# Optimization experiments

Hardware: AMD Instinct MI355X
Metric: run time of the kernel (lower is better)

The kernel has to match this reference:

```python
import jax, jax.numpy as jnp
import numpy as np

B, P, M, C = 64, 8732, 16, 81
THRESHOLD = 0.5
NEG_POS_RATIO = 3
ALPHA = 1.0  # config.reg_weights
EPS = 1e-7


def cxcy_to_xy(c):
    return jnp.concatenate([c[..., :2] - c[..., 2:] / 2.0,
                            c[..., :2] + c[..., 2:] / 2.0], axis=-1)


def _rand_boxes_cxcy(key, shape):
    k1, k2 = jax.random.split(key)
    cxcy = jax.random.uniform(k1, shape + (2,), minval=0.2, maxval=0.8)
    wh = jax.random.uniform(k2, shape + (2,), minval=0.05, maxval=0.35)
    return jnp.concatenate([cxcy, wh], axis=-1)


def setup_inputs() -> dict:
    key = jax.random.key(0)
    ks = jax.random.split(key, 5)
    predicted_locs = cxcy_to_xy(_rand_boxes_cxcy(ks[0], (B, P)))          # valid corner boxes
    predicted_scores = jax.random.normal(ks[1], (B, P, C), dtype=jnp.float32)
    boxes = jnp.clip(cxcy_to_xy(_rand_boxes_cxcy(ks[2], (B, M))), 0.0, 1.0)  # GT corner boxes
    labels = jax.random.randint(ks[3], (B, M), 1, C)                       # object labels (1..C-1)
    priors_cxcy = _rand_boxes_cxcy(ks[4], (P,))
    return {"predicted_locs": predicted_locs, "predicted_scores": predicted_scores,
            "boxes": boxes, "labels": labels, "priors_cxcy": priors_cxcy}


def jaccard(a, b):
    # a: [M,4], b: [P,4] corner boxes -> [M,P] IoU
    lt = jnp.maximum(a[:, None, :2], b[None, :, :2])
    rb = jnp.minimum(a[:, None, 2:], b[None, :, 2:])
    wh = jnp.clip(rb - lt, 0.0)
    inter = wh[..., 0] * wh[..., 1]
    area_a = (a[:, 2] - a[:, 0]) * (a[:, 3] - a[:, 1])
    area_b = (b[:, 2] - b[:, 0]) * (b[:, 3] - b[:, 1])
    return inter / (area_a[:, None] + area_b[None, :] - inter)


def diou_loss(b1, b2):
    # corner boxes, elementwise over leading dims -> per-box loss 1 - DIoU
    lt = jnp.maximum(b1[..., :2], b2[..., :2])
    rb = jnp.minimum(b1[..., 2:], b2[..., 2:])
    wh = jnp.clip(rb - lt, 0.0)
    inter = wh[..., 0] * wh[..., 1]
    area1 = (b1[..., 2] - b1[..., 0]) * (b1[..., 3] - b1[..., 1])
    area2 = (b2[..., 2] - b2[..., 0]) * (b2[..., 3] - b2[..., 1])
    iou = inter / (area1 + area2 - inter + EPS)
    c1 = (b1[..., :2] + b1[..., 2:]) / 2.0
    c2 = (b2[..., :2] + b2[..., 2:]) / 2.0
    inter_diag = jnp.sum((c1 - c2) ** 2, axis=-1)
    enc_lt = jnp.minimum(b1[..., :2], b2[..., :2])
    enc_rb = jnp.maximum(b1[..., 2:], b2[..., 2:])
    outer_diag = jnp.sum((enc_rb - enc_lt) ** 2, axis=-1)
    dious = jnp.clip(iou - inter_diag / (outer_diag + EPS), -1.0, 1.0)
    return 1.0 - dious


def reference(predicted_locs, predicted_scores, boxes, labels, priors_cxcy):
    priors_xy = cxcy_to_xy(priors_cxcy)

    def assign(boxes_i, labels_i):
        overlap = jaccard(boxes_i, priors_xy)              # [M, P]
        ovl_prior = overlap.max(axis=0)                    # best overlap per prior
        obj_prior = overlap.argmax(axis=0)                 # best object per prior
        ovl_obj = overlap.max(axis=1)                      # best overlap per object
        prior_obj = overlap.argmax(axis=1)                 # best prior per object
        valid = ovl_obj > 0
        j_idx = jnp.cumsum(valid.astype(jnp.int32)) - 1    # index within filtered list (faithful)
        idx = jnp.where(valid, prior_obj, P)               # P -> dropped (out of bounds)
        ovl_prior = ovl_prior.at[idx].set(1.0, mode='drop')
        obj_prior = obj_prior.at[idx].set(j_idx, mode='drop')
        lab = labels_i[obj_prior]
        label_pos = jnp.where(ovl_prior < THRESHOLD, 0, lab)
        label_neg = jnp.where(ovl_prior < THRESHOLD - 0.1, -1, lab)
        return label_pos, label_neg

    true_classes, true_neg_classes = jax.vmap(assign)(boxes, labels)  # [B,P] each
    positive = true_classes > 0                                        # [B,P]
    pos_f = positive.astype(jnp.float32)
    n_pos_total = jnp.sum(pos_f)

    # Localization loss: DIoU(pred_pos, pred_pos) with reduce='mean' (faithful to source)
    per_box = diou_loss(predicted_locs, predicted_locs)                # [B,P]
    loc_loss = jnp.sum(per_box * pos_f) / jnp.maximum(n_pos_total, 1.0)

    # Confidence loss: per-prior CE + hard-negative mining (neg_pos_ratio)
    logp = jax.nn.log_softmax(predicted_scores, axis=-1)
    conf_all = -jnp.take_along_axis(logp, true_classes[..., None], axis=-1)[..., 0]  # [B,P]
    conf_pos_sum = jnp.sum(conf_all * pos_f)
    conf_neg = jnp.where(positive, 0.0, conf_all)
    conf_neg_sorted = -jnp.sort(-conf_neg, axis=-1)                    # descending
    n_hard = NEG_POS_RATIO * jnp.sum(positive, axis=1)                 # [B]
    hard_mask = (jnp.arange(P)[None, :] < n_hard[:, None]).astype(jnp.float32)
    conf_loss = (jnp.sum(conf_neg_sorted * hard_mask) + conf_pos_sum) / n_pos_total

    return conf_loss + ALPHA * loc_loss
```

## Files before the change

### kernel.cpp

```cpp
#include <hip/hip_runtime.h>
#include <math.h>

#define B_ 64
#define P_ 8732
#define M_ 16
#define C_ 81
#define THRESH 0.5f
#define EPS_ 1e-7f

#define CE_GRID 768
#define NBLK_CE CE_GRID
#define ROWS_PER_CHUNK 64
#define NCHUNKS ((B_ * P_) / ROWS_PER_CHUNK)
#define CHUNK_F4 (ROWS_PER_CHUNK * C_ / 4)

__global__ __launch_bounds__(1024) void assign_kernel(
    const float* __restrict__ boxes,
    const int*   __restrict__ labels,
    const float* __restrict__ priors,
    int*         __restrict__ true_classes,
    int*         __restrict__ n_pos)
{
    const int b = blockIdx.x;
    const int tid = threadIdx.x;
    const int lane = tid & 63;
    const int wv = tid >> 6;

    __shared__ float s_ovl[P_];
    __shared__ unsigned char s_obj[P_];
    __shared__ float s_bx[M_][4];
    __shared__ float s_barea[M_];
    __shared__ int   s_lab[M_];
    __shared__ float s_wv[M_][16];
    __shared__ int   s_wp[M_][16];
    __shared__ float s_ovl_obj[M_];
    __shared__ int   s_prior_obj[M_];
    __shared__ int   s_cnt[16];

    if (tid < M_*4) ((float*)s_bx)[tid] = boxes[b*M_*4 + tid];
    if (tid < M_)   s_lab[tid] = labels[b*M_ + tid];
    __syncthreads();
    if (tid < M_)
        s_barea[tid] = (s_bx[tid][2]-s_bx[tid][0])*(s_bx[tid][3]-s_bx[tid][1]);
    __syncthreads();

    float bestv[M_]; int bestp[M_];
    #pragma unroll
    for (int m = 0; m < M_; ++m) { bestv[m] = -1.0f; bestp[m] = 0x7fffffff; }

    for (int p = tid; p < P_; p += 1024) {
        float4 pc = ((const float4*)priors)[p];
        float px1 = pc.x - pc.z*0.5f, py1 = pc.y - pc.w*0.5f;
        float px2 = pc.x + pc.z*0.5f, py2 = pc.y + pc.w*0.5f;
        float parea = (px2-px1)*(py2-py1);
        float bv = -1.0f; int bm = 0;
        #pragma unroll
        for (int m = 0; m < M_; ++m) {
            float ix1 = fmaxf(s_bx[m][0], px1);
            float iy1 = fmaxf(s_bx[m][1], py1);
            float ix2 = fminf(s_bx[m][2], px2);
            float iy2 = fminf(s_bx[m][3], py2);
            float iw = fmaxf(ix2-ix1, 0.0f);
            float ih = fmaxf(iy2-iy1, 0.0f);
            float inter = iw*ih;
            float iou = inter / (s_barea[m] + parea - inter);
            if (iou > bv) { bv = iou; bm = m; }
            if (iou > bestv[m]) { bestv[m] = iou; bestp[m] = p; }
        }
        s_ovl[p] = bv;
        s_obj[p] = (unsigned char)bm;
    }

    #pragma unroll
    for (int m = 0; m < M_; ++m) {
        float v = bestv[m]; int p = bestp[m];
        #pragma unroll
        for (int o = 32; o; o >>= 1) {
            float v2 = __shfl_xor(v, o);
            int   p2 = __shfl_xor(p, o);
            if (v2 > v || (v2 == v && p2 < p)) { v = v2; p = p2; }
        }
        if (lane == 0) { s_wv[m][wv] = v; s_wp[m][wv] = p; }
    }
    __syncthreads();

    if (tid < M_) {
        float v = s_wv[tid][0]; int p = s_wp[tid][0];
        #pragma unroll
        for (int w = 1; w < 16; ++w) {
            float v2 = s_wv[tid][w]; int p2 = s_wp[tid][w];
            if (v2 > v || (v2 == v && p2 < p)) { v = v2; p = p2; }
        }
        s_ovl_obj[tid] = v; s_prior_obj[tid] = p;
    }
    __syncthreads();

    if (tid == 0) {
        int cnt = 0;
        for (int m = 0; m < M_; ++m) {
            if (s_ovl_obj[m] > 0.0f) {
                int p = s_prior_obj[m];
                s_ovl[p] = 1.0f;
                s_obj[p] = (unsigned char)cnt;
                cnt++;
            }
        }
    }
    __syncthreads();

    int cpos = 0;
    for (int p = tid; p < P_; p += 1024) {
        int tc = 0;
        if (!(s_ovl[p] < THRESH)) tc = s_lab[s_obj[p]];
        true_classes[(size_t)b*P_ + p] = tc;
        cpos += (tc > 0);
    }
    #pragma unroll
    for (int o = 32; o; o >>= 1) cpos += __shfl_xor(cpos, o);
    if (lane == 0) s_cnt[wv] = cpos;
    __syncthreads();
    if (tid == 0) {
        int t = 0;
        #pragma unroll
        for (int w = 0; w < 16; ++w) t += s_cnt[w];
        n_pos[b] = t;
    }
}

__device__ __forceinline__ void ce_stage_load(const float4* __restrict__ scores4,
                                              int c, int tid, float4 st4[6])
{
    const float4* src = scores4 + (size_t)c * CHUNK_F4;
    #pragma unroll
    for (int k = 0; k < 5; ++k) st4[k] = src[k*256 + tid];
    if (tid < 16) st4[5] = src[1280 + tid];
}

__device__ __forceinline__ void ce_stage_write(float* bufp, int tid,
                                               const float4 st4[6])
{
    float4* dst = (float4*)bufp;
    #pragma unroll
    for (int k = 0; k < 5; ++k) dst[k*256 + tid] = st4[k];
    if (tid < 16) dst[1280 + tid] = st4[5];
}

__global__ __launch_bounds__(256) void ce_loc_kernel(
    const float* __restrict__ scores,
    const float* __restrict__ locs,
    const int*   __restrict__ tcls,
    float*       __restrict__ conf_neg,
    float*       __restrict__ blk_pos,
    float*       __restrict__ blk_loc)
{
    const int tid  = threadIdx.x;
    const int lane = tid & 63;
    const int wv   = tid >> 6;
    const int s    = lane & 3;
    const int rl   = (lane >> 2) + wv * 16;

    __shared__ __attribute__((aligned(16))) float s_buf[2][ROWS_PER_CHUNK * C_];
    __shared__ float s_red[4][2];

    const int cnt   = (s == 0) ? 21 : 20;
    const int cbase = (s == 0) ? 0  : (1 + 20 * s);

    float p_acc = 0.f, l_acc = 0.f;
    const float4* scores4 = (const float4*)scores;

    float4 st4[6];

    int c0 = blockIdx.x;
    ce_stage_load(scores4, c0, tid, st4);
    ce_stage_write(s_buf[0], tid, st4);
    __syncthreads();

    int buf = 0;
    for (int c = c0; c < NCHUNKS; c += CE_GRID) {
        const int cn = c + CE_GRID;
        const bool have_next = (cn < NCHUNKS);
        if (have_next) ce_stage_load(scores4, cn, tid, st4);

        const float* rowp = &s_buf[buf][rl * C_ + cbase];
        float x[21];
        float mx = -INFINITY;
        #pragma unroll
        for (int k = 0; k < 21; ++k) {
            if (k < cnt) { x[k] = rowp[k]; mx = fmaxf(mx, x[k]); }
            else x[k] = -INFINITY;
        }
        mx = fmaxf(mx, __shfl_xor(mx, 1));
        mx = fmaxf(mx, __shfl_xor(mx, 2));

        const int row = c * ROWS_PER_CHUNK + rl;
        const int t = tcls[row];

        float e = 0.f, stv = 0.f;
        #pragma unroll
        for (int k = 0; k < 21; ++k) {
            e += __expf(x[k] - mx);
            if ((cbase + k == t) && (k < cnt)) stv = x[k];
        }
        e   += __shfl_xor(e, 1);   e   += __shfl_xor(e, 2);
        stv += __shfl_xor(stv, 1); stv += __shfl_xor(stv, 2);

        if (s == 0) {
            float conf = mx + __logf(e) - stv;
            if (t > 0) {
                conf_neg[row] = 0.f;
                p_acc += conf;
                float4 bx = ((const float4*)locs)[row];
                float w = bx.z - bx.x, h = bx.w - bx.y;
                float iw = fmaxf(w, 0.f), ih = fmaxf(h, 0.f);
                float inter = iw * ih;
                float area  = w * h;
                float iou   = inter / (area + area - inter + EPS_);
                float diou  = fminf(fmaxf(iou, -1.f), 1.f);
                l_acc += 1.f - diou;
            } else {
                conf_neg[row] = fmaxf(conf, 0.f);
            }
        }

        if (have_next) ce_stage_write(s_buf[buf ^ 1], tid, st4);
        __syncthreads();
        buf ^= 1;
    }

    #pragma unroll
    for (int o = 32; o; o >>= 1) {
        p_acc += __shfl_xor(p_acc, o);
        l_acc += __shfl_xor(l_acc, o);
    }
    if (lane == 0) { s_red[wv][0] = p_acc; s_red[wv][1] = l_acc; }
    __syncthreads();
    if (tid == 0) {
        blk_pos[blockIdx.x] = s_red[0][0] + s_red[1][0] + s_red[2][0] + s_red[3][0];
        blk_loc[blockIdx.x] = s_red[0][1] + s_red[1][1] + s_red[2][1] + s_red[3][1];
    }
}

__global__ __launch_bounds__(1024) void topk_kernel(
    const float* __restrict__ conf_neg,
    const int*   __restrict__ n_pos,
    float*       __restrict__ hard)
{
    const int b = blockIdx.x;
    const int tid = threadIdx.x;
    const int lane = tid & 63;
    const int wv = tid >> 6;

    __shared__ float s_v[P_];
    __shared__ int   s_hist[16][256];
    __shared__ int   s_cg[257];
    __shared__ int   s_sel;
    __shared__ int   s_t[16];
    __shared__ float s_f[16];

    for (int i = tid; i < P_; i += 1024) s_v[i] = conf_neg[(size_t)b*P_ + i];
    int k = 3 * n_pos[b];
    if (k <= 0) { if (tid == 0) hard[b] = 0.f; return; }
    if (k > P_) k = P_;
    __syncthreads();

    const unsigned masks[4]  = {0u, 0xFF800000u, 0xFFFF8000u, 0xFFFFFF80u};
    const int      shifts[4] = {23, 15, 7, 0};

    unsigned prefix = 0u;
    int k_rem = k;

    for (int rd = 0; rd < 4; ++rd) {
        const unsigned hm = masks[rd];
        const int sh = shifts[rd];

        ((int*)s_hist)[tid] = 0;
        ((int*)s_hist)[tid + 1024] = 0;
        ((int*)s_hist)[tid + 2048] = 0;
        ((int*)s_hist)[tid + 3072] = 0;
        __syncthreads();

        for (int i = tid; i < P_; i += 1024) {
            unsigned u = __float_as_uint(s_v[i]);
            if ((u & hm) == prefix)
                atomicAdd(&s_hist[wv][(u >> sh) & 0xFF], 1);
        }
        __syncthreads();

        if (wv == 0) {
            int carry = 0;
            for (int cbin = 3; cbin >= 0; --cbin) {
                int bin = cbin * 64 + lane;
                int tot = 0;
                #pragma unroll
                for (int w = 0; w < 16; ++w) tot += s_hist[w][bin];
                #pragma unroll
                for (int o = 1; o < 64; o <<= 1) {
                    int v = __shfl_down(tot, o);
                    if (lane + o < 64) tot += v;
                }
                int cg = tot + carry;
                s_cg[bin] = cg;
                carry = __shfl(cg, 0);
            }
            if (lane == 0) s_cg[256] = 0;
        }
        __syncthreads();

        if (tid < 256) {
            if (s_cg[tid] >= k_rem && s_cg[tid + 1] < k_rem) s_sel = tid;
        }
        __syncthreads();

        const int bsel = s_sel;
        k_rem -= s_cg[bsel + 1];
        prefix |= (unsigned)bsel << sh;
        __syncthreads();
    }

    const float tval = __uint_as_float(prefix);

    float sum = 0.f; int cgt = 0;
    for (int i = tid; i < P_; i += 1024) {
        float v = s_v[i];
        if (v > tval) { sum += v; cgt++; }
    }
    #pragma unroll
    for (int o = 32; o; o >>= 1) { sum += __shfl_xor(sum, o); cgt += __shfl_xor(cgt, o); }
    if (lane == 0) { s_f[wv] = sum; s_t[wv] = cgt; }
    __syncthreads();
    if (tid == 0) {
        float ssum = 0.f; int cc = 0;
        #pragma unroll
        for (int w = 0; w < 16; ++w) { ssum += s_f[w]; cc += s_t[w]; }
        hard[b] = ssum + (float)(k - cc) * tval;
    }
}

__global__ __launch_bounds__(256) void final_kernel(
    const float* __restrict__ blk_pos,
    const float* __restrict__ blk_loc,
    const float* __restrict__ hard,
    const int*   __restrict__ n_pos,
    float*       __restrict__ out)
{
    const int tid = threadIdx.x;
    const int lane = tid & 63;
    const int wv = tid >> 6;
    __shared__ double sd[4][4];

    double p = 0.0, l = 0.0, h = 0.0, np = 0.0;
    for (int i = tid; i < NBLK_CE; i += 256) { p += blk_pos[i]; l += blk_loc[i]; }
    if (tid < B_) { h = hard[tid]; np = (double)n_pos[tid]; }

    #pragma unroll
    for (int o = 32; o; o >>= 1) {
        p += __shfl_xor(p, o); l += __shfl_xor(l, o);
        h += __shfl_xor(h, o); np += __shfl_xor(np, o);
    }
    if (lane == 0) { sd[wv][0] = p; sd[wv][1] = l; sd[wv][2] = h; sd[wv][3] = np; }
    __syncthreads();
    if (tid == 0) {
        double tp = 0, tl = 0, th = 0, tn = 0;
        #pragma unroll
        for (int w = 0; w < 4; ++w) { tp += sd[w][0]; tl += sd[w][1]; th += sd[w][2]; tn += sd[w][3]; }
        double conf_loss = (th + tp) / tn;
        double loc_loss  = tl / fmax(tn, 1.0);
        out[0] = (float)(conf_loss + 1.0 * loc_loss);
    }
}

extern "C" void kernel_launch(void* const* d_in, const int* in_sizes, int n_in,
                              void* d_out, int out_size, void* d_ws, size_t ws_size,
                              hipStream_t stream) {
    const float* predicted_locs   = (const float*)d_in[0];
    const float* predicted_scores = (const float*)d_in[1];
    const float* boxes            = (const float*)d_in[2];
    const int*   labels           = (const int*)d_in[3];
    const float* priors           = (const float*)d_in[4];
    float* out = (float*)d_out;

    char* ws = (char*)d_ws;
    size_t off = 0;
    int*    true_classes = (int*)(ws + off);   off += sizeof(int)   * (size_t)B_ * P_;
    float*  conf_neg     = (float*)(ws + off); off += sizeof(float) * (size_t)B_ * P_;
    int*    n_pos        = (int*)(ws + off);   off += sizeof(int)   * B_;
    float*  hard         = (float*)(ws + off); off += sizeof(float) * B_;
    float*  blk_pos      = (float*)(ws + off); off += sizeof(float) * NBLK_CE;
    float*  blk_loc      = (float*)(ws + off); off += sizeof(float) * NBLK_CE;

    assign_kernel<<<B_, 1024, 0, stream>>>(boxes, labels, priors,
                                           true_classes, n_pos);
    ce_loc_kernel<<<CE_GRID, 256, 0, stream>>>(predicted_scores, predicted_locs,
                                               true_classes, conf_neg,
                                               blk_pos, blk_loc);
    topk_kernel<<<B_, 1024, 0, stream>>>(conf_neg, n_pos, hard);
    final_kernel<<<1, 256, 0, stream>>>(blk_pos, blk_loc, hard, n_pos, out);
}
```

Before: 379.2 us.

## Use one-chunk-per-block CE with direct global-to-LDS loads and fuse final reduction

The CE kernel switches from a persistent 768-block double-buffered loop to one block per 64-row chunk (8732 blocks), staging scores with global_load_lds straight into shared memory and declaring a minimum of 6 blocks per CU. The final reduction kernel is removed. Its work moves into the topk kernel through a last-block-done atomic counter, which is reset in assign_kernel. The top-k load is also vectorised to float4. This aims to cut register staging and one kernel launch, at the cost of a larger per-block partial array and more block scheduling overhead.

After: 361.2 us. 1.05x faster.

```diff
diff --git a/kernel.cpp b/kernel.cpp
--- a/kernel.cpp
+++ b/kernel.cpp
@@ -8,8 +8,6 @@
 #define THRESH 0.5f
 #define EPS_ 1e-7f
 
-#define CE_GRID 768
-#define NBLK_CE CE_GRID
 #define ROWS_PER_CHUNK 64
 #define NCHUNKS ((B_ * P_) / ROWS_PER_CHUNK)
 #define CHUNK_F4 (ROWS_PER_CHUNK * C_ / 4)
@@ -19,12 +17,15 @@
     const int*   __restrict__ labels,
     const float* __restrict__ priors,
     int*         __restrict__ true_classes,
-    int*         __restrict__ n_pos)
+    int*         __restrict__ n_pos,
+    int*         __restrict__ done_ctr)
 {
     const int b = blockIdx.x;
     const int tid = threadIdx.x;
     const int lane = tid & 63;
     const int wv = tid >> 6;
+
+    if (b == 0 && tid == 0) *done_ctr = 0;
 
     __shared__ float s_ovl[P_];
     __shared__ unsigned char s_obj[P_];
@@ -127,25 +128,7 @@
     }
 }
 
-__device__ __forceinline__ void ce_stage_load(const float4* __restrict__ scores4,
-                                              int c, int tid, float4 st4[6])
-{
-    const float4* src = scores4 + (size_t)c * CHUNK_F4;
-    #pragma unroll
-    for (int k = 0; k < 5; ++k) st4[k] = src[k*256 + tid];
-    if (tid < 16) st4[5] = src[1280 + tid];
-}
-
-__device__ __forceinline__ void ce_stage_write(float* bufp, int tid,
-                                               const float4 st4[6])
-{
-    float4* dst = (float4*)bufp;
-    #pragma unroll
-    for (int k = 0; k < 5; ++k) dst[k*256 + tid] = st4[k];
-    if (tid < 16) dst[1280 + tid] = st4[5];
-}
-
-__global__ __launch_bounds__(256) void ce_loc_kernel(
+__global__ __launch_bounds__(256, 6) void ce_loc_kernel(
     const float* __restrict__ scores,
     const float* __restrict__ locs,
     const int*   __restrict__ tcls,
@@ -153,78 +136,72 @@
     float*       __restrict__ blk_pos,
     float*       __restrict__ blk_loc)
 {
+    const int c    = blockIdx.x;
     const int tid  = threadIdx.x;
     const int lane = tid & 63;
     const int wv   = tid >> 6;
     const int s    = lane & 3;
     const int rl   = (lane >> 2) + wv * 16;
 
-    __shared__ __attribute__((aligned(16))) float s_buf[2][ROWS_PER_CHUNK * C_];
+    __shared__ __attribute__((aligned(16))) float s_buf[ROWS_PER_CHUNK * C_];
     __shared__ float s_red[4][2];
+
+    const float4* src4 = (const float4*)scores + (size_t)c * CHUNK_F4;
+    float4*       dst4 = (float4*)s_buf;
+
+    #pragma unroll
+    for (int k = 0; k < 5; ++k) {
+        __builtin_amdgcn_global_load_lds(
+            (const __attribute__((address_space(1))) void*)(src4 + k*256 + tid),
+            (__attribute__((address_space(3))) void*)(dst4 + k*256 + wv*64),
+            16, 0, 0);
+    }
+    if (tid < 16) dst4[1280 + tid] = src4[1280 + tid];
+
+    const int row = c * ROWS_PER_CHUNK + rl;
+    const int t = tcls[row];
+    __syncthreads();
 
     const int cnt   = (s == 0) ? 21 : 20;
     const int cbase = (s == 0) ? 0  : (1 + 20 * s);
 
+    const float* rowp = &s_buf[rl * C_ + cbase];
+    float x[21];
+    float mx = -INFINITY;
+    #pragma unroll
+    for (int k = 0; k < 21; ++k) {
+        if (k < cnt) { x[k] = rowp[k]; mx = fmaxf(mx, x[k]); }
+        else x[k] = -INFINITY;
+    }
+    mx = fmaxf(mx, __shfl_xor(mx, 1));
+    mx = fmaxf(mx, __shfl_xor(mx, 2));
+
+    float e = 0.f, stv = 0.f;
+    #pragma unroll
+    for (int k = 0; k < 21; ++k) {
+        e += __expf(x[k] - mx);
+        if ((cbase + k == t) && (k < cnt)) stv = x[k];
+    }
+    e   += __shfl_xor(e, 1);   e   += __shfl_xor(e, 2);
+    stv += __shfl_xor(stv, 1); stv += __shfl_xor(stv, 2);
+
     float p_acc = 0.f, l_acc = 0.f;
-    const float4* scores4 = (const float4*)scores;
-
-    float4 st4[6];
-
-    int c0 = blockIdx.x;
-    ce_stage_load(scores4, c0, tid, st4);
-    ce_stage_write(s_buf[0], tid, st4);
-    __syncthreads();
-
-    int buf = 0;
-    for (int c = c0; c < NCHUNKS; c += CE_GRID) {
-        const int cn = c + CE_GRID;
-        const bool have_next = (cn < NCHUNKS);
-        if (have_next) ce_stage_load(scores4, cn, tid, st4);
-
-        const float* rowp = &s_buf[buf][rl * C_ + cbase];
-        float x[21];
-        float mx = -INFINITY;
-        #pragma unroll
-        for (int k = 0; k < 21; ++k) {
-            if (k < cnt) { x[k] = rowp[k]; mx = fmaxf(mx, x[k]); }
-            else x[k] = -INFINITY;
-        }
-        mx = fmaxf(mx, __shfl_xor(mx, 1));
-        mx = fmaxf(mx, __shfl_xor(mx, 2));
-
-        const int row = c * ROWS_PER_CHUNK + rl;
-        const int t = tcls[row];
-
-        float e = 0.f, stv = 0.f;
-        #pragma unroll
-        for (int k = 0; k < 21; ++k) {
-            e += __expf(x[k] - mx);
-            if ((cbase + k == t) && (k < cnt)) stv = x[k];
-        }
-        e   += __shfl_xor(e, 1);   e   += __shfl_xor(e, 2);
-        stv += __shfl_xor(stv, 1); stv += __shfl_xor(stv, 2);
-
-        if (s == 0) {
-            float conf = mx + __logf(e) - stv;
-            if (t > 0) {
-                conf_neg[row] = 0.f;
-                p_acc += conf;
-                float4 bx = ((const float4*)locs)[row];
-                float w = bx.z - bx.x, h = bx.w - bx.y;
-                float iw = fmaxf(w, 0.f), ih = fmaxf(h, 0.f);
-                float inter = iw * ih;
-                float area  = w * h;
-                float iou   = inter / (area + area - inter + EPS_);
-                float diou  = fminf(fmaxf(iou, -1.f), 1.f);
-                l_acc += 1.f - diou;
-            } else {
-                conf_neg[row] = fmaxf(conf, 0.f);
-            }
-        }
-
-        if (have_next) ce_stage_write(s_buf[buf ^ 1], tid, st4);
-        __syncthreads();
-        buf ^= 1;
+    if (s == 0) {
+        float conf = mx + __logf(e) - stv;
+        if (t > 0) {
+            conf_neg[row] = 0.f;
+            p_acc = conf;
+            float4 bx = ((const float4*)locs)[row];
+            float w = bx.z - bx.x, h = bx.w - bx.y;
+            float iw = fmaxf(w, 0.f), ih = fmaxf(h, 0.f);
+            float inter = iw * ih;
+            float area  = w * h;
+            float iou   = inter / (area + area - inter + EPS_);
+            float diou  = fminf(fmaxf(iou, -1.f), 1.f);
+            l_acc = 1.f - diou;
+        } else {
+            conf_neg[row] = fmaxf(conf, 0.f);
+        }
     }
 
     #pragma unroll
@@ -235,15 +212,19 @@
     if (lane == 0) { s_red[wv][0] = p_acc; s_red[wv][1] = l_acc; }
     __syncthreads();
     if (tid == 0) {
-        blk_pos[blockIdx.x] = s_red[0][0] + s_red[1][0] + s_red[2][0] + s_red[3][0];
-        blk_loc[blockIdx.x] = s_red[0][1] + s_red[1][1] + s_red[2][1] + s_red[3][1];
+        blk_pos[c] = s_red[0][0] + s_red[1][0] + s_red[2][0] + s_red[3][0];
+        blk_loc[c] = s_red[0][1] + s_red[1][1] + s_red[2][1] + s_red[3][1];
     }
 }
 
 __global__ __launch_bounds__(1024) void topk_kernel(
     const float* __restrict__ conf_neg,
     const int*   __restrict__ n_pos,
-    float*       __restrict__ hard)
+    const float* __restrict__ blk_pos,
+    const float* __restrict__ blk_loc,
+    float*       __restrict__ hard,
+    int*         __restrict__ done_ctr,
+    float*       __restrict__ out)
 {
     const int b = blockIdx.x;
     const int tid = threadIdx.x;
@@ -256,116 +237,123 @@
     __shared__ int   s_sel;
     __shared__ int   s_t[16];
     __shared__ float s_f[16];
-
-    for (int i = tid; i < P_; i += 1024) s_v[i] = conf_neg[(size_t)b*P_ + i];
+    __shared__ int   s_last;
+    __shared__ double sd[16][4];
+
+    const float4* cn4 = (const float4*)(conf_neg + (size_t)b * P_);
+    for (int i = tid; i < P_/4; i += 1024) ((float4*)s_v)[i] = cn4[i];
+
     int k = 3 * n_pos[b];
-    if (k <= 0) { if (tid == 0) hard[b] = 0.f; return; }
     if (k > P_) k = P_;
-    __syncthreads();
-
-    const unsigned masks[4]  = {0u, 0xFF800000u, 0xFFFF8000u, 0xFFFFFF80u};
-    const int      shifts[4] = {23, 15, 7, 0};
-
-    unsigned prefix = 0u;
-    int k_rem = k;
-
-    for (int rd = 0; rd < 4; ++rd) {
-        const unsigned hm = masks[rd];
-        const int sh = shifts[rd];
-
-        ((int*)s_hist)[tid] = 0;
-        ((int*)s_hist)[tid + 1024] = 0;
-        ((int*)s_hist)[tid + 2048] = 0;
-        ((int*)s_hist)[tid + 3072] = 0;
+
+    float hsum = 0.f;
+    if (k > 0) {
         __syncthreads();
 
+        const unsigned masks[4]  = {0u, 0xFF800000u, 0xFFFF8000u, 0xFFFFFF80u};
+        const int      shifts[4] = {23, 15, 7, 0};
+
+        unsigned prefix = 0u;
+        int k_rem = k;
+
+        for (int rd = 0; rd < 4; ++rd) {
+            const unsigned hm = masks[rd];
+            const int sh = shifts[rd];
+
+            ((int*)s_hist)[tid] = 0;
+            ((int*)s_hist)[tid + 1024] = 0;
+            ((int*)s_hist)[tid + 2048] = 0;
+            ((int*)s_hist)[tid + 3072] = 0;
+            __syncthreads();
+
+            for (int i = tid; i < P_; i += 1024) {
+                unsigned u = __float_as_uint(s_v[i]);
+                if ((u & hm) == prefix)
+                    atomicAdd(&s_hist[wv][(u >> sh) & 0xFF], 1);
+            }
+            __syncthreads();
+
+            if (wv == 0) {
+                int carry = 0;
+                for (int cbin = 3; cbin >= 0; --cbin) {
+                    int bin = cbin * 64 + lane;
+                    int tot = 0;
+                    #pragma unroll
+                    for (int w = 0; w < 16; ++w) tot += s_hist[w][bin];
+                    #pragma unroll
+                    for (int o = 1; o < 64; o <<= 1) {
+                        int v = __shfl_down(tot, o);
+                        if (lane + o < 64) tot += v;
+                    }
+                    int cg = tot + carry;
+                    s_cg[bin] = cg;
+                    carry = __shfl(cg, 0);
+                }
+                if (lane == 0) s_cg[256] = 0;
+            }
+            __syncthreads();
+
+            if (tid < 256) {
+                if (s_cg[tid] >= k_rem && s_cg[tid + 1] < k_rem) s_sel = tid;
+            }
+            __syncthreads();
+
+            const int bsel = s_sel;
+            k_rem -= s_cg[bsel + 1];
+            prefix |= (unsigned)bsel << sh;
+            __syncthreads();
+        }
+
+        const float tval = __uint_as_float(prefix);
+
+        float sum = 0.f; int cgt = 0;
         for (int i = tid; i < P_; i += 1024) {
-            unsigned u = __float_as_uint(s_v[i]);
-            if ((u & hm) == prefix)
-                atomicAdd(&s_hist[wv][(u >> sh) & 0xFF], 1);
-        }
+            float v = s_v[i];
+            if (v > tval) { sum += v; cgt++; }
+        }
+        #pragma unroll
+        for (int o = 32; o; o >>= 1) { sum += __shfl_xor(sum, o); cgt += __shfl_xor(cgt, o); }
+        if (lane == 0) { s_f[wv] = sum; s_t[wv] = cgt; }
         __syncthreads();
-
-        if (wv == 0) {
-            int carry = 0;
-            for (int cbin = 3; cbin >= 0; --cbin) {
-                int bin = cbin * 64 + lane;
-                int tot = 0;
-                #pragma unroll
-                for (int w = 0; w < 16; ++w) tot += s_hist[w][bin];
-                #pragma unroll
-                for (int o = 1; o < 64; o <<= 1) {
-                    int v = __shfl_down(tot, o);
-                    if (lane + o < 64) tot += v;
-                }
-                int cg = tot + carry;
-                s_cg[bin] = cg;
-                carry = __shfl(cg, 0);
-            }
-            if (lane == 0) s_cg[256] = 0;
-        }
+        if (tid == 0) {
+            float ssum = 0.f; int cc = 0;
+            #pragma unroll
+            for (int w = 0; w < 16; ++w) { ssum += s_f[w]; cc += s_t[w]; }
+            hsum = ssum + (float)(k - cc) * tval;
+        }
+    }
+
+    if (tid == 0) {
+        atomicExch(&hard[b], hsum);
+        __threadfence();
+        s_last = (atomicAdd(done_ctr, 1) == B_ - 1) ? 1 : 0;
+    }
+    __syncthreads();
+
+    if (s_last) {
+        __threadfence();
+        double p = 0.0, l = 0.0;
+        for (int i = tid; i < NCHUNKS; i += 1024) { p += blk_pos[i]; l += blk_loc[i]; }
+        double h = 0.0, np = 0.0;
+        if (tid < B_) {
+            h  = (double)atomicAdd(&hard[tid], 0.0f);
+            np = (double)n_pos[tid];
+        }
+        #pragma unroll
+        for (int o = 32; o; o >>= 1) {
+            p += __shfl_xor(p, o); l += __shfl_xor(l, o);
+            h += __shfl_xor(h, o); np += __shfl_xor(np, o);
+        }
+        if (lane == 0) { sd[wv][0] = p; sd[wv][1] = l; sd[wv][2] = h; sd[wv][3] = np; }
         __syncthreads();
-
-        if (tid < 256) {
-            if (s_cg[tid] >= k_rem && s_cg[tid + 1] < k_rem) s_sel = tid;
-        }
-        __syncthreads();
-
-        const int bsel = s_sel;
-        k_rem -= s_cg[bsel + 1];
-        prefix |= (unsigned)bsel << sh;
-        __syncthreads();
-    }
-
-    const float tval = __uint_as_float(prefix);
-
-    float sum = 0.f; int cgt = 0;
-    for (int i = tid; i < P_; i += 1024) {
-        float v = s_v[i];
-        if (v > tval) { sum += v; cgt++; }
-    }
-    #pragma unroll
-    for (int o = 32; o; o >>= 1) { sum += __shfl_xor(sum, o); cgt += __shfl_xor(cgt, o); }
-    if (lane == 0) { s_f[wv] = sum; s_t[wv] = cgt; }
-    __syncthreads();
-    if (tid == 0) {
-        float ssum = 0.f; int cc = 0;
-        #pragma unroll
-        for (int w = 0; w < 16; ++w) { ssum += s_f[w]; cc += s_t[w]; }
-        hard[b] = ssum + (float)(k - cc) * tval;
-    }
-}
-
-__global__ __launch_bounds__(256) void final_kernel(
-    const float* __restrict__ blk_pos,
-    const float* __restrict__ blk_loc,
-    const float* __restrict__ hard,
-    const int*   __restrict__ n_pos,
-    float*       __restrict__ out)
-{
-    const int tid = threadIdx.x;
-    const int lane = tid & 63;
-    const int wv = tid >> 6;
-    __shared__ double sd[4][4];
-
-    double p = 0.0, l = 0.0, h = 0.0, np = 0.0;
-    for (int i = tid; i < NBLK_CE; i += 256) { p += blk_pos[i]; l += blk_loc[i]; }
-    if (tid < B_) { h = hard[tid]; np = (double)n_pos[tid]; }
-
-    #pragma unroll
-    for (int o = 32; o; o >>= 1) {
-        p += __shfl_xor(p, o); l += __shfl_xor(l, o);
-        h += __shfl_xor(h, o); np += __shfl_xor(np, o);
-    }
-    if (lane == 0) { sd[wv][0] = p; sd[wv][1] = l; sd[wv][2] = h; sd[wv][3] = np; }
-    __syncthreads();
-    if (tid == 0) {
-        double tp = 0, tl = 0, th = 0, tn = 0;
-        #pragma unroll
-        for (int w = 0; w < 4; ++w) { tp += sd[w][0]; tl += sd[w][1]; th += sd[w][2]; tn += sd[w][3]; }
-        double conf_loss = (th + tp) / tn;
-        double loc_loss  = tl / fmax(tn, 1.0);
-        out[0] = (float)(conf_loss + 1.0 * loc_loss);
+        if (tid == 0) {
+            double tp = 0, tl = 0, th = 0, tn = 0;
+            #pragma unroll
+            for (int w = 0; w < 16; ++w) { tp += sd[w][0]; tl += sd[w][1]; th += sd[w][2]; tn += sd[w][3]; }
+            double conf_loss = (th + tp) / tn;
+            double loc_loss  = tl / fmax(tn, 1.0);
+            out[0] = (float)(conf_loss + 1.0 * loc_loss);
+        }
     }
 }
 
@@ -383,16 +371,17 @@
     size_t off = 0;
     int*    true_classes = (int*)(ws + off);   off += sizeof(int)   * (size_t)B_ * P_;
     float*  conf_neg     = (float*)(ws + off); off += sizeof(float) * (size_t)B_ * P_;
+    float*  blk_pos      = (float*)(ws + off); off += sizeof(float) * NCHUNKS;
+    float*  blk_loc      = (float*)(ws + off); off += sizeof(float) * NCHUNKS;
+    float*  hard         = (float*)(ws + off); off += sizeof(float) * B_;
     int*    n_pos        = (int*)(ws + off);   off += sizeof(int)   * B_;
-    float*  hard         = (float*)(ws + off); off += sizeof(float) * B_;
-    float*  blk_pos      = (float*)(ws + off); off += sizeof(float) * NBLK_CE;
-    float*  blk_loc      = (float*)(ws + off); off += sizeof(float) * NBLK_CE;
+    int*    done_ctr     = (int*)(ws + off);   off += sizeof(int)   * 4;
 
     assign_kernel<<<B_, 1024, 0, stream>>>(boxes, labels, priors,
-                                           true_classes, n_pos);
-    ce_loc_kernel<<<CE_GRID, 256, 0, stream>>>(predicted_scores, predicted_locs,
+                                           true_classes, n_pos, done_ctr);
+    ce_loc_kernel<<<NCHUNKS, 256, 0, stream>>>(predicted_scores, predicted_locs,
                                                true_classes, conf_neg,
                                                blk_pos, blk_loc);
-    topk_kernel<<<B_, 1024, 0, stream>>>(conf_neg, n_pos, hard);
-    final_kernel<<<1, 256, 0, stream>>>(blk_pos, blk_loc, hard, n_pos, out);
+    topk_kernel<<<B_, 1024, 0, stream>>>(conf_neg, n_pos, blk_pos, blk_loc,
+                                         hard, done_ctr, out);
 }
```
